# Kernel optimization log

Measured on AMD Instinct MI355X. Metric: run time of the kernel, lower is better.

The kernel has to match this reference:

```python
import jax, jax.numpy as jnp
import numpy as np

EMBED = 1024
HEADS = 16
HEAD_DIM = EMBED // HEADS
N, L = 2, 2048


def setup_inputs() -> dict:
    key = jax.random.key(0)
    ks = jax.random.split(key, 9)
    s = 0.02
    return {
        "values": jax.random.normal(ks[0], (N, L, EMBED), jnp.float32),
        "key": jax.random.normal(ks[1], (N, L, EMBED), jnp.float32),
        "query": jax.random.normal(ks[2], (N, L, EMBED), jnp.float32),
        "mask": jnp.ones((N, 1, 1, L), jnp.int32),
        "Wv": jax.random.normal(ks[3], (HEAD_DIM, HEAD_DIM), jnp.float32) * s,
        "Wk": jax.random.normal(ks[4], (HEAD_DIM, HEAD_DIM), jnp.float32) * s,
        "Wq": jax.random.normal(ks[5], (HEAD_DIM, HEAD_DIM), jnp.float32) * s,
        "bq": jax.random.normal(ks[6], (HEAD_DIM,), jnp.float32) * s,
        "Wo": jax.random.normal(ks[7], (EMBED, EMBED), jnp.float32) * s,
        "bo": jax.random.normal(ks[8], (EMBED,), jnp.float32) * s,
    }


def reference(values, key, query, mask, Wv, Wk, Wq, bq, Wo, bo):
    n, q_len, E = query.shape
    D = Wv.shape[0]
    H = E // D
    # split heads: (N, len, H, D)
    v = values.reshape(n, -1, H, D)
    k = key.reshape(n, -1, H, D)
    q = query.reshape(n, q_len, H, D)
    # per-head linear projections (torch Linear: x @ W.T [+ b])
    v = jnp.einsum("nlhd,ed->nlhe", v, Wv)
    k = jnp.einsum("nlhd,ed->nlhe", k, Wk)
    q = jnp.einsum("nlhd,ed->nlhe", q, Wq) + bq
    # scores: (N, H, q_len, k_len)
    energy = jnp.einsum("nqhd,nkhd->nhqk", q, k)
    energy = jnp.where(mask == 0, jnp.float32(-1e20), energy)
    # NOTE: original scales by sqrt(embed_size), not sqrt(head_dim)
    attn = jax.nn.softmax(energy / jnp.sqrt(jnp.float32(E)), axis=-1)
    out = jnp.einsum("nhqk,nkhd->nqhd", attn, v).reshape(n, q_len, E)
    return out @ Wo.T + bo
```

## Files before the change

### kernel.cpp

```cpp
#include <hip/hip_runtime.h>
#include <hip/hip_bf16.h>
#include <string.h>

#define NB   2
#define SEQ  2048
#define EMB  1024
#define NH   16
#define HD   64
#define QSCALE 0.045084219f

typedef __attribute__((ext_vector_type(8))) short short8;
typedef __attribute__((ext_vector_type(4))) float f32x4;

#define MFMA(a, b, c) __builtin_amdgcn_mfma_f32_16x16x32_bf16(a, b, c, 0, 0, 0)
#define EXP2(x) __builtin_amdgcn_exp2f(x)

__device__ __forceinline__ unsigned short f2bf(float x) {
    union { float f; unsigned u; } v; v.f = x;
    unsigned r = v.u + 0x7fffu + ((v.u >> 16) & 1u);
    return (unsigned short)(r >> 16);
}
__device__ __forceinline__ unsigned packbf2(float a, float b) {
    __hip_bfloat162 h = __float22bfloat162_rn(make_float2(a, b));
    unsigned u; memcpy(&u, &h, 4);
    return u;
}
__device__ __forceinline__ void gload16(const void* g, void* l) {
    __builtin_amdgcn_global_load_lds(
        (const __attribute__((address_space(1))) void*)g,
        (__attribute__((address_space(3))) void*)l, 16, 0, 0);
}

__global__ __launch_bounds__(256) void cvt_kernel(
    const float* __restrict__ Wo, const float* __restrict__ Wq,
    const float* __restrict__ Wk, const float* __restrict__ Wv,
    const int* __restrict__ mask,
    unsigned short* __restrict__ Wob, unsigned short* __restrict__ Wqb,
    unsigned short* __restrict__ Wkb, unsigned short* __restrict__ Wvb,
    unsigned short* __restrict__ Mb)
{
    const int b = blockIdx.x, tid = threadIdx.x;
    if (b < 1024) {
        int idx = b * 256 + tid;
        float4 w = ((const float4*)Wo)[idx];
        uint2 p; p.x = packbf2(w.x, w.y); p.y = packbf2(w.z, w.w);
        ((uint2*)Wob)[idx] = p;
    } else if (b < 1027) {
        const float* W = (b == 1024) ? Wq : (b == 1025) ? Wk : Wv;
        unsigned short* Wb = (b == 1024) ? Wqb : (b == 1025) ? Wkb : Wvb;
        #pragma unroll
        for (int i = 0; i < 4; ++i) {
            int idx = tid + i * 256;
            float4 w = ((const float4*)W)[idx];
            uint2 p; p.x = packbf2(w.x, w.y); p.y = packbf2(w.z, w.w);
            ((uint2*)Wb)[idx] = p;
        }
    } else {
        #pragma unroll
        for (int i = 0; i < 16; ++i) {
            int idx = tid + i * 256;
            Mb[idx] = mask[idx] ? (unsigned short)0x3F80 : (unsigned short)0;
        }
    }
}

__global__ __launch_bounds__(256) void qkv_kernel(
    const float* __restrict__ Qin, const float* __restrict__ Kin,
    const float* __restrict__ Vin,
    const unsigned short* __restrict__ Wqb, const unsigned short* __restrict__ Wkb,
    const unsigned short* __restrict__ Wvb, const float* __restrict__ bq,
    const int* __restrict__ mask,
    unsigned short* __restrict__ Qp, unsigned short* __restrict__ Kp,
    unsigned short* __restrict__ Vtp)
{
    const int lt = blockIdx.x;
    const int h  = blockIdx.y;
    const int tz = blockIdx.z;
    const int t  = tz >> 1, n = tz & 1;

    const float* X; const unsigned short* Wb;
    if (t == 0)      { X = Qin; Wb = Wqb; }
    else if (t == 1) { X = Kin; Wb = Wkb; }
    else             { X = Vin; Wb = Wvb; }

    __shared__ __align__(16) unsigned short sX[128][70];
    __shared__ __align__(16) unsigned short sT[64][136];

    const int tid = threadIdx.x, wave = tid >> 6, lane = tid & 63;
    const int ln = lane & 15, quad = lane >> 4;

    #pragma unroll
    for (int i = 0; i < 8; ++i) {
        int flat = tid + i * 256;
        int r = flat >> 4, c4 = flat & 15;
        float4 xv = *(const float4*)(X + ((size_t)(n * SEQ + lt * 128 + r)) * EMB + h * HD + c4 * 4);
        uint2 xp; xp.x = packbf2(xv.x, xv.y); xp.y = packbf2(xv.z, xv.w);
        *(uint2*)&sX[r][c4 * 4] = xp;
    }
    short8 wf0[4], wf1[4];
    #pragma unroll
    for (int nt = 0; nt < 4; ++nt) {
        wf0[nt] = *(const short8*)(Wb + (nt * 16 + ln) * HD + quad * 8);
        wf1[nt] = *(const short8*)(Wb + (nt * 16 + ln) * HD + 32 + quad * 8);
    }
    __syncthreads();

    f32x4 acc[2][4];
    #pragma unroll
    for (int set = 0; set < 2; ++set) {
        short8 af0 = *(const short8*)&sX[wave * 32 + set * 16 + ln][quad * 8];
        short8 af1 = *(const short8*)&sX[wave * 32 + set * 16 + ln][32 + quad * 8];
        #pragma unroll
        for (int nt = 0; nt < 4; ++nt) {
            f32x4 a = {0.f, 0.f, 0.f, 0.f};
            a = MFMA(af0, wf0[nt], a);
            a = MFMA(af1, wf1[nt], a);
            acc[set][nt] = a;
        }
    }

    if (t == 0) {
        #pragma unroll
        for (int nt = 0; nt < 4; ++nt) {
            float bb = bq[nt * 16 + ln];
            #pragma unroll
            for (int set = 0; set < 2; ++set)
                #pragma unroll
                for (int a = 0; a < 4; ++a)
                    acc[set][nt][a] = (acc[set][nt][a] + bb) * QSCALE;
        }
    }

    if (t < 2) {
        unsigned short* Out = (t == 0) ? Qp : Kp;
        #pragma unroll
        for (int set = 0; set < 2; ++set)
            #pragma unroll
            for (int a = 0; a < 4; ++a) {
                size_t row = (size_t)((n * NH + h) * SEQ + lt * 128 + wave * 32 + set * 16 + quad * 4 + a);
                #pragma unroll
                for (int nt = 0; nt < 4; ++nt)
                    Out[row * HD + nt * 16 + ln] = f2bf(acc[set][nt][a]);
            }
    } else {
        #pragma unroll
        for (int set = 0; set < 2; ++set)
            #pragma unroll
            for (int a = 0; a < 4; ++a) {
                int l = lt * 128 + wave * 32 + set * 16 + quad * 4 + a;
                if (mask[n * SEQ + l] == 0) {
                    #pragma unroll
                    for (int nt = 0; nt < 4; ++nt) acc[set][nt][a] = 0.f;
                }
            }
        #pragma unroll
        for (int set = 0; set < 2; ++set)
            #pragma unroll
            for (int nt = 0; nt < 4; ++nt)
                #pragma unroll
                for (int a = 0; a < 4; ++a)
                    sT[nt * 16 + ln][wave * 32 + set * 16 + quad * 4 + a] = f2bf(acc[set][nt][a]);
        __syncthreads();
        #pragma unroll
        for (int i = 0; i < 4; ++i) {
            int flat = tid + i * 256;
            int r = flat >> 4, c8 = flat & 15;
            *(float4*)(Vtp + ((size_t)((n * NH + h) * HD + r)) * SEQ + lt * 128 + c8 * 8) =
                *(const float4*)&sT[r][c8 * 8];
        }
    }
}

__global__ __launch_bounds__(256, 2) void flash_kernel(
    const unsigned short* __restrict__ Qp, const unsigned short* __restrict__ Kp,
    const unsigned short* __restrict__ Vtp, const unsigned short* __restrict__ Mb,
    unsigned short* __restrict__ A )
{
    const int nh = blockIdx.x;
    const int qt = blockIdx.y;
    const int n  = nh >> 4, h = nh & 15;

    const int tid  = threadIdx.x;
    const int wave = tid >> 6, lane = tid & 63;
    const int ln   = lane & 15, quad = lane >> 4;
    const int ln7  = lane & 7;

    __shared__ __align__(16) unsigned short Kb[2][64 * 64];
    __shared__ __align__(16) unsigned short Vb[2][64 * 64];
    __shared__ __align__(16) unsigned short sP[4][32 * 64];
    unsigned short* sPw = sP[wave];

    const unsigned short* Qb = Qp + ((size_t)nh * SEQ + qt * 128 + wave * 32) * HD;
    short8 qf[2][2];
    #pragma unroll
    for (int set = 0; set < 2; ++set) {
        qf[set][0] = *(const short8*)(Qb + (set * 16 + ln) * HD + quad * 8);
        qf[set][1] = *(const short8*)(Qb + (set * 16 + ln) * HD + 32 + quad * 8);
    }

    const unsigned short* Kg = Kp  + (size_t)nh * SEQ * HD;
    const unsigned short* Vg = Vtp + (size_t)nh * HD * SEQ;
    const unsigned short* mk = Mb + n * SEQ;

    const int kx0 = ((quad)     ^ ln7) << 3;
    const int kx1 = ((quad + 4) ^ ln7) << 3;
    const int pw0 = ((quad >> 1) ^ ln7) << 3;
    const int pwb = (quad & 1) * 4;

    const int r8  = lane >> 3;
    const int swz = ((lane & 7) ^ r8) << 3;

    f32x4 o[2][4];
    #pragma unroll
    for (int s2 = 0; s2 < 2; ++s2)
        #pragma unroll
        for (int dt = 0; dt < 4; ++dt) o[s2][dt] = (f32x4){0.f, 0.f, 0.f, 0.f};
    f32x4 ol[2] = {(f32x4){0.f, 0.f, 0.f, 0.f}, (f32x4){0.f, 0.f, 0.f, 0.f}};

    #define STAGE(buf, kt_) do {                                                  \
        const unsigned short* kg_ = Kg + ((size_t)((kt_) * 64 + wave * 16 + r8)) * HD + swz; \
        const unsigned short* vg_ = Vg + ((size_t)(wave * 16 + r8)) * SEQ + (kt_) * 64 + swz; \
        unsigned short* kl_ = &Kb[buf][wave * 16 * 64];                           \
        unsigned short* vl_ = &Vb[buf][wave * 16 * 64];                           \
        gload16(kg_,            kl_);                                             \
        gload16(kg_ + 8 * HD,   kl_ + 8 * 64);                                    \
        gload16(vg_,            vl_);                                             \
        gload16(vg_ + 8 * SEQ,  vl_ + 8 * 64);                                    \
    } while (0)

    #define COMPUTE(BUF, KT) do {                                                 \
        short8 mf0 = *(const short8*)(mk + (KT) * 64 + quad * 8);                 \
        short8 mf1 = *(const short8*)(mk + (KT) * 64 + 32 + quad * 8);            \
        _Pragma("unroll")                                                         \
        for (int nt = 0; nt < 4; ++nt) {                                          \
            short8 kf0 = *(const short8*)&Kb[BUF][(nt * 16 + ln) * 64 + kx0];     \
            short8 kf1 = *(const short8*)&Kb[BUF][(nt * 16 + ln) * 64 + kx1];     \
            _Pragma("unroll")                                                     \
            for (int set = 0; set < 2; ++set) {                                   \
                f32x4 z = {0.f, 0.f, 0.f, 0.f};                                   \
                z = MFMA(kf0, qf[set][0], z);                                     \
                z = MFMA(kf1, qf[set][1], z);                                     \
                float p0 = EXP2(z[0]);                                            \
                float p1 = EXP2(z[1]);                                            \
                float p2 = EXP2(z[2]);                                            \
                float p3 = EXP2(z[3]);                                            \
                uint2 w; w.x = packbf2(p0, p1); w.y = packbf2(p2, p3);            \
                *(uint2*)&sPw[(set * 16 + ln) * 64 + (pw0 ^ (nt * 2 << 3)) + pwb] = w; \
            }                                                                     \
        }                                                                         \
        asm volatile("s_waitcnt lgkmcnt(0)" ::: "memory");                        \
        short8 pf[2][2];                                                          \
        _Pragma("unroll")                                                         \
        for (int set = 0; set < 2; ++set) {                                       \
            pf[set][0] = *(const short8*)&sPw[(set * 16 + ln) * 64 + kx0];        \
            pf[set][1] = *(const short8*)&sPw[(set * 16 + ln) * 64 + kx1];        \
        }                                                                         \
        _Pragma("unroll")                                                         \
        for (int set = 0; set < 2; ++set) {                                       \
            ol[set] = MFMA(pf[set][0], mf0, ol[set]);                             \
            ol[set] = MFMA(pf[set][1], mf1, ol[set]);                             \
        }                                                                         \
        _Pragma("unroll")                                                         \
        for (int dt = 0; dt < 4; ++dt) {                                          \
            short8 vf0 = *(const short8*)&Vb[BUF][(dt * 16 + ln) * 64 + kx0];     \
            short8 vf1 = *(const short8*)&Vb[BUF][(dt * 16 + ln) * 64 + kx1];     \
            _Pragma("unroll")                                                     \
            for (int set = 0; set < 2; ++set) {                                   \
                o[set][dt] = MFMA(pf[set][0], vf0, o[set][dt]);                   \
                o[set][dt] = MFMA(pf[set][1], vf1, o[set][dt]);                   \
            }                                                                     \
        }                                                                         \
    } while (0)

    STAGE(0, 0);
    __syncthreads();

    #pragma unroll 1
    for (int kt = 0; kt < SEQ / 64; kt += 2) {
        STAGE(1, kt + 1);
        COMPUTE(0, kt);
        __syncthreads();
        if (kt + 2 < SEQ / 64) STAGE(0, kt + 2);
        COMPUTE(1, kt + 1);
        __syncthreads();
    }
    #undef STAGE
    #undef COMPUTE

    #pragma unroll
    for (int set = 0; set < 2; ++set)
        #pragma unroll
        for (int a = 0; a < 4; ++a) {
            float inv = 1.0f / ol[set][a];
            size_t row = (size_t)(n * SEQ + qt * 128 + wave * 32 + set * 16 + quad * 4 + a);
            #pragma unroll
            for (int dt = 0; dt < 4; ++dt)
                A[row * EMB + h * HD + dt * 16 + ln] = f2bf(o[set][dt][a] * inv);
        }
}

__global__ __launch_bounds__(256) void outproj_kernel(
    const unsigned short* __restrict__ A, const unsigned short* __restrict__ Wob,
    const float* __restrict__ bo, float* __restrict__ Out)
{
    const int ct = blockIdx.x;
    const int rt = blockIdx.y;

    const int tid  = threadIdx.x;
    const int wave = tid >> 6, lane = tid & 63;
    const int ln   = lane & 15, quad = lane >> 4;
    const int ln7  = lane & 7;
    const int wm   = wave >> 1, wn = wave & 1;

    __shared__ __align__(16) unsigned short sA[2][128 * 64];
    __shared__ __align__(16) unsigned short sB[2][128 * 64];

    const int r8  = lane >> 3;
    const int swz = ((lane & 7) ^ r8) << 3;

    f32x4 acc[4][4];
    #pragma unroll
    for (int i = 0; i < 4; ++i)
        #pragma unroll
        for (int j = 0; j < 4; ++j) acc[i][j] = (f32x4){0.f, 0.f, 0.f, 0.f};

    #define STAGE(buf, kc_) do {                                                  \
        _Pragma("unroll")                                                         \
        for (int sub = 0; sub < 4; ++sub) {                                       \
            int rloc = wave * 32 + sub * 8;                                       \
            gload16(A   + (size_t)(rt * 128 + rloc + r8) * EMB + (kc_) * 64 + swz,\
                    &sA[buf][rloc * 64]);                                         \
            gload16(Wob + (size_t)(ct * 128 + rloc + r8) * EMB + (kc_) * 64 + swz,\
                    &sB[buf][rloc * 64]);                                         \
        }                                                                         \
    } while (0)

    #define COMPUTE(BUF) do {                                                     \
        _Pragma("unroll")                                                         \
        for (int ks = 0; ks < 2; ++ks) {                                          \
            short8 af[4], bf[4];                                                  \
            _Pragma("unroll")                                                     \
            for (int i = 0; i < 4; ++i)                                           \
                af[i] = *(const short8*)&sA[BUF][(wm * 64 + i * 16 + ln) * 64     \
                                                + (((ks * 4 + quad) ^ ln7) << 3)];\
            _Pragma("unroll")                                                     \
            for (int j = 0; j < 4; ++j)                                           \
                bf[j] = *(const short8*)&sB[BUF][(wn * 64 + j * 16 + ln) * 64     \
                                                + (((ks * 4 + quad) ^ ln7) << 3)];\
            _Pragma("unroll")                                                     \
            for (int i = 0; i < 4; ++i)                                           \
                _Pragma("unroll")                                                 \
                for (int j = 0; j < 4; ++j)                                       \
                    acc[i][j] = MFMA(af[i], bf[j], acc[i][j]);                    \
        }                                                                         \
    } while (0)

    STAGE(0, 0);
    __syncthreads();

    #pragma unroll 1
    for (int kc = 0; kc < EMB / 64; kc += 2) {
        STAGE(1, kc + 1);
        COMPUTE(0);
        __syncthreads();
        if (kc + 2 < EMB / 64) STAGE(0, kc + 2);
        COMPUTE(1);
        __syncthreads();
    }
    #undef STAGE
    #undef COMPUTE

    #pragma unroll
    for (int j = 0; j < 4; ++j) {
        int col = ct * 128 + wn * 64 + j * 16 + ln;
        float bb = bo[col];
        #pragma unroll
        for (int i = 0; i < 4; ++i)
            #pragma unroll
            for (int a = 0; a < 4; ++a) {
                size_t row = (size_t)(rt * 128 + wm * 64 + i * 16 + quad * 4 + a);
                Out[row * EMB + col] = acc[i][j][a] + bb;
            }
    }
}

extern "C" void kernel_launch(void* const* d_in, const int* in_sizes, int n_in,
                              void* d_out, int out_size, void* d_ws, size_t ws_size,
                              hipStream_t stream) {
    const float* values = (const float*)d_in[0];
    const float* key_   = (const float*)d_in[1];
    const float* query  = (const float*)d_in[2];
    const int*   mask   = (const int*)d_in[3];
    const float* Wv     = (const float*)d_in[4];
    const float* Wk     = (const float*)d_in[5];
    const float* Wq     = (const float*)d_in[6];
    const float* bq     = (const float*)d_in[7];
    const float* Wo     = (const float*)d_in[8];
    const float* bo     = (const float*)d_in[9];
    float* out = (float*)d_out;

    const size_t NHLD = (size_t)NB * NH * SEQ * HD;

    unsigned short* ws = (unsigned short*)d_ws;
    unsigned short* Qp    = ws;
    unsigned short* Kp    = ws + NHLD;
    unsigned short* Vtp   = ws + 2 * NHLD;
    unsigned short* Aattn = ws + 3 * NHLD;
    unsigned short* Wob   = ws + 4 * NHLD;
    unsigned short* Wqb   = Wob + (size_t)EMB * EMB;
    unsigned short* Wkb   = Wqb + HD * HD;
    unsigned short* Wvb   = Wkb + HD * HD;
    unsigned short* Mb    = Wvb + HD * HD;

    cvt_kernel<<<dim3(1028), 256, 0, stream>>>(
        Wo, Wq, Wk, Wv, mask, Wob, Wqb, Wkb, Wvb, Mb);
    qkv_kernel<<<dim3(SEQ / 128, NH, 3 * NB), 256, 0, stream>>>(
        query, key_, values, Wqb, Wkb, Wvb, bq, mask, Qp, Kp, Vtp);
    flash_kernel<<<dim3(NB * NH, SEQ / 128), 256, 0, stream>>>(
        Qp, Kp, Vtp, Mb, Aattn);
    outproj_kernel<<<dim3(EMB / 128, NB * SEQ / 128), 256, 0, stream>>>(
        Aattn, Wob, bo, out);
}
```

Baseline: 185.4 us.

## Fuse weight/mask conversion into QKV kernel, stage Q/K stores, raise MFMA priority

Removes the separate cvt_kernel launch. Its Wo and mask conversion moves into the first blocks of qkv_kernel, and the small per-head weights are now converted from fp32 directly inside each QKV block. The Q/K outputs are first staged through shared memory so they can be written as coalesced 16-byte stores, replacing scattered 2-byte stores. The flash kernel raises wave priority around its PV MFMA section. The aim is to save a launch and improve store efficiency, at the cost of extra per-block weight conversion work and more shared memory.

```diff
diff --git a/kernel.cpp b/kernel.cpp
--- a/kernel.cpp
+++ b/kernel.cpp
@@ -25,51 +25,25 @@
     unsigned u; memcpy(&u, &h, 4);
     return u;
 }
+__device__ __forceinline__ short8 pack8(float4 a, float4 b) {
+    unsigned u[4];
+    u[0] = packbf2(a.x, a.y); u[1] = packbf2(a.z, a.w);
+    u[2] = packbf2(b.x, b.y); u[3] = packbf2(b.z, b.w);
+    short8 r; memcpy(&r, u, 16); return r;
+}
 __device__ __forceinline__ void gload16(const void* g, void* l) {
     __builtin_amdgcn_global_load_lds(
         (const __attribute__((address_space(1))) void*)g,
         (__attribute__((address_space(3))) void*)l, 16, 0, 0);
 }
 
-__global__ __launch_bounds__(256) void cvt_kernel(
-    const float* __restrict__ Wo, const float* __restrict__ Wq,
-    const float* __restrict__ Wk, const float* __restrict__ Wv,
-    const int* __restrict__ mask,
-    unsigned short* __restrict__ Wob, unsigned short* __restrict__ Wqb,
-    unsigned short* __restrict__ Wkb, unsigned short* __restrict__ Wvb,
-    unsigned short* __restrict__ Mb)
-{
-    const int b = blockIdx.x, tid = threadIdx.x;
-    if (b < 1024) {
-        int idx = b * 256 + tid;
-        float4 w = ((const float4*)Wo)[idx];
-        uint2 p; p.x = packbf2(w.x, w.y); p.y = packbf2(w.z, w.w);
-        ((uint2*)Wob)[idx] = p;
-    } else if (b < 1027) {
-        const float* W = (b == 1024) ? Wq : (b == 1025) ? Wk : Wv;
-        unsigned short* Wb = (b == 1024) ? Wqb : (b == 1025) ? Wkb : Wvb;
-        #pragma unroll
-        for (int i = 0; i < 4; ++i) {
-            int idx = tid + i * 256;
-            float4 w = ((const float4*)W)[idx];
-            uint2 p; p.x = packbf2(w.x, w.y); p.y = packbf2(w.z, w.w);
-            ((uint2*)Wb)[idx] = p;
-        }
-    } else {
-        #pragma unroll
-        for (int i = 0; i < 16; ++i) {
-            int idx = tid + i * 256;
-            Mb[idx] = mask[idx] ? (unsigned short)0x3F80 : (unsigned short)0;
-        }
-    }
-}
-
 __global__ __launch_bounds__(256) void qkv_kernel(
     const float* __restrict__ Qin, const float* __restrict__ Kin,
     const float* __restrict__ Vin,
-    const unsigned short* __restrict__ Wqb, const unsigned short* __restrict__ Wkb,
-    const unsigned short* __restrict__ Wvb, const float* __restrict__ bq,
-    const int* __restrict__ mask,
+    const float* __restrict__ Wqf, const float* __restrict__ Wkf,
+    const float* __restrict__ Wvf, const float* __restrict__ bq,
+    const int* __restrict__ mask, const float* __restrict__ Wo,
+    unsigned short* __restrict__ Wob, unsigned short* __restrict__ Mb,
     unsigned short* __restrict__ Qp, unsigned short* __restrict__ Kp,
     unsigned short* __restrict__ Vtp)
 {
@@ -77,17 +51,30 @@
     const int h  = blockIdx.y;
     const int tz = blockIdx.z;
     const int t  = tz >> 1, n = tz & 1;
-
-    const float* X; const unsigned short* Wb;
-    if (t == 0)      { X = Qin; Wb = Wqb; }
-    else if (t == 1) { X = Kin; Wb = Wkb; }
-    else             { X = Vin; Wb = Wvb; }
-
-    __shared__ __align__(16) unsigned short sX[128][70];
-    __shared__ __align__(16) unsigned short sT[64][136];
+    const int bid = blockIdx.x + 16 * blockIdx.y + 256 * blockIdx.z;
 
     const int tid = threadIdx.x, wave = tid >> 6, lane = tid & 63;
     const int ln = lane & 15, quad = lane >> 4;
+
+    if (bid < 1024) {
+        int idx = bid * 256 + tid;
+        float4 w = ((const float4*)Wo)[idx];
+        uint2 p; p.x = packbf2(w.x, w.y); p.y = packbf2(w.z, w.w);
+        ((uint2*)Wob)[idx] = p;
+    } else if (bid < 1040) {
+        int idx = (bid - 1024) * 256 + tid;
+        Mb[idx] = mask[idx] ? (unsigned short)0x3F80 : (unsigned short)0;
+    }
+
+    const float* X; const float* Wf;
+    if (t == 0)      { X = Qin; Wf = Wqf; }
+    else if (t == 1) { X = Kin; Wf = Wkf; }
+    else             { X = Vin; Wf = Wvf; }
+
+    __shared__ __align__(16) unsigned short sX[128][70];
+    __shared__ __align__(16) unsigned short sPool[128 * 72];
+    unsigned short (*sT)[136] = (unsigned short(*)[136])sPool;
+    unsigned short (*sM)[72]  = (unsigned short(*)[72])sPool;
 
     #pragma unroll
     for (int i = 0; i < 8; ++i) {
@@ -100,8 +87,11 @@
     short8 wf0[4], wf1[4];
     #pragma unroll
     for (int nt = 0; nt < 4; ++nt) {
-        wf0[nt] = *(const short8*)(Wb + (nt * 16 + ln) * HD + quad * 8);
-        wf1[nt] = *(const short8*)(Wb + (nt * 16 + ln) * HD + 32 + quad * 8);
+        const float* wr = Wf + (nt * 16 + ln) * HD;
+        wf0[nt] = pack8(*(const float4*)(wr + quad * 8),
+                        *(const float4*)(wr + quad * 8 + 4));
+        wf1[nt] = pack8(*(const float4*)(wr + 32 + quad * 8),
+                        *(const float4*)(wr + 32 + quad * 8 + 4));
     }
     __syncthreads();
 
@@ -132,16 +122,24 @@
     }
 
     if (t < 2) {
+        #pragma unroll
+        for (int set = 0; set < 2; ++set)
+            #pragma unroll
+            for (int nt = 0; nt < 4; ++nt)
+                #pragma unroll
+                for (int a = 0; a < 4; ++a)
+                    sM[wave * 32 + set * 16 + quad * 4 + a][nt * 16 + ln] =
+                        f2bf(acc[set][nt][a]);
+        __syncthreads();
         unsigned short* Out = (t == 0) ? Qp : Kp;
-        #pragma unroll
-        for (int set = 0; set < 2; ++set)
-            #pragma unroll
-            for (int a = 0; a < 4; ++a) {
-                size_t row = (size_t)((n * NH + h) * SEQ + lt * 128 + wave * 32 + set * 16 + quad * 4 + a);
-                #pragma unroll
-                for (int nt = 0; nt < 4; ++nt)
-                    Out[row * HD + nt * 16 + ln] = f2bf(acc[set][nt][a]);
-            }
+        size_t base = ((size_t)((n * NH + h) * SEQ + lt * 128)) * HD;
+        #pragma unroll
+        for (int i = 0; i < 4; ++i) {
+            int idx = tid + i * 256;
+            int r = idx >> 3, c8 = idx & 7;
+            *(float4*)(Out + base + (size_t)r * HD + c8 * 8) =
+                *(const float4*)&sM[r][c8 * 8];
+        }
     } else {
         #pragma unroll
         for (int set = 0; set < 2; ++set)
@@ -249,6 +247,7 @@
             }                                                                     \
         }                                                                         \
         asm volatile("s_waitcnt lgkmcnt(0)" ::: "memory");                        \
+        __builtin_amdgcn_s_setprio(1);                                            \
         short8 pf[2][2];                                                          \
         _Pragma("unroll")                                                         \
         for (int set = 0; set < 2; ++set) {                                       \
@@ -270,6 +269,7 @@
                 o[set][dt] = MFMA(pf[set][1], vf1, o[set][dt]);                   \
             }                                                                     \
         }                                                                         \
+        __builtin_amdgcn_s_setprio(0);                                            \
     } while (0)
 
     STAGE(0, 0);
@@ -407,15 +407,10 @@
     unsigned short* Vtp   = ws + 2 * NHLD;
     unsigned short* Aattn = ws + 3 * NHLD;
     unsigned short* Wob   = ws + 4 * NHLD;
-    unsigned short* Wqb   = Wob + (size_t)EMB * EMB;
-    unsigned short* Wkb   = Wqb + HD * HD;
-    unsigned short* Wvb   = Wkb + HD * HD;
-    unsigned short* Mb    = Wvb + HD * HD;
-
-    cvt_kernel<<<dim3(1028), 256, 0, stream>>>(
-        Wo, Wq, Wk, Wv, mask, Wob, Wqb, Wkb, Wvb, Mb);
+    unsigned short* Mb    = Wob + (size_t)EMB * EMB;
+
     qkv_kernel<<<dim3(SEQ / 128, NH, 3 * NB), 256, 0, stream>>>(
-        query, key_, values, Wqb, Wkb, Wvb, bq, mask, Qp, Kp, Vtp);
+        query, key_, values, Wq, Wk, Wv, bq, mask, Wo, Wob, Mb, Qp, Kp, Vtp);
     flash_kernel<<<dim3(NB * NH, SEQ / 128), 256, 0, stream>>>(
         Qp, Kp, Vtp, Mb, Aattn);
     outproj_kernel<<<dim3(EMB / 128, NB * SEQ / 128), 256, 0, stream>>>(
```

Result: no change. 188.3 us (+1.5%).

## Software-pipeline flash loop: overlap P·V of previous tile with QK of next

Applied to the files above, without the earlier changes.

The attention inner loop is split into QK (scores, exp, write P to LDS), VFLOAD (V fragments into registers) and PV (mask-sum and P·V MFMAs) stages. It is restructured so each iteration runs PV for the previous key tile while computing QK for the next, with double-buffered P scratch in LDS and two register sets of V fragments. This removes the explicit LDS wait between writing P and reading it back, and exposes independent MFMA and exp work to hide latency. The cost is higher register use (two sets of V fragments) and double the LDS for P, which could reduce occupancy or cause spills.

```diff
diff --git a/kernel.cpp b/kernel.cpp
--- a/kernel.cpp
+++ b/kernel.cpp
@@ -187,8 +187,9 @@
 
     __shared__ __align__(16) unsigned short Kb[2][64 * 64];
     __shared__ __align__(16) unsigned short Vb[2][64 * 64];
-    __shared__ __align__(16) unsigned short sP[4][32 * 64];
-    unsigned short* sPw = sP[wave];
+    __shared__ __align__(16) unsigned short sP[2][4][32 * 64];
+    unsigned short* const sPw0 = &sP[0][wave][0];
+    unsigned short* const sPw1 = &sP[1][wave][0];
 
     const unsigned short* Qb = Qp + ((size_t)nh * SEQ + qt * 128 + wave * 32) * HD;
     short8 qf[2][2];
@@ -216,6 +217,8 @@
         #pragma unroll
         for (int dt = 0; dt < 4; ++dt) o[s2][dt] = (f32x4){0.f, 0.f, 0.f, 0.f};
     f32x4 ol[2] = {(f32x4){0.f, 0.f, 0.f, 0.f}, (f32x4){0.f, 0.f, 0.f, 0.f}};
+
+    short8 vfA[4][2], vfB[4][2];
 
     #define STAGE(buf, kt_) do {                                                  \
         const unsigned short* kg_ = Kg + ((size_t)((kt_) * 64 + wave * 16 + r8)) * HD + swz; \
@@ -228,13 +231,11 @@
         gload16(vg_ + 8 * SEQ,  vl_ + 8 * 64);                                    \
     } while (0)
 
-    #define COMPUTE(BUF, KT) do {                                                 \
-        short8 mf0 = *(const short8*)(mk + (KT) * 64 + quad * 8);                 \
-        short8 mf1 = *(const short8*)(mk + (KT) * 64 + 32 + quad * 8);            \
+    #define QK(SPW, KBUF, KT) do {                                               \
         _Pragma("unroll")                                                         \
         for (int nt = 0; nt < 4; ++nt) {                                          \
-            short8 kf0 = *(const short8*)&Kb[BUF][(nt * 16 + ln) * 64 + kx0];     \
-            short8 kf1 = *(const short8*)&Kb[BUF][(nt * 16 + ln) * 64 + kx1];     \
+            short8 kf0 = *(const short8*)&Kb[KBUF][(nt * 16 + ln) * 64 + kx0];    \
+            short8 kf1 = *(const short8*)&Kb[KBUF][(nt * 16 + ln) * 64 + kx1];    \
             _Pragma("unroll")                                                     \
             for (int set = 0; set < 2; ++set) {                                   \
                 f32x4 z = {0.f, 0.f, 0.f, 0.f};                                   \
@@ -245,15 +246,27 @@
                 float p2 = EXP2(z[2]);                                            \
                 float p3 = EXP2(z[3]);                                            \
                 uint2 w; w.x = packbf2(p0, p1); w.y = packbf2(p2, p3);            \
-                *(uint2*)&sPw[(set * 16 + ln) * 64 + (pw0 ^ (nt * 2 << 3)) + pwb] = w; \
+                *(uint2*)&(SPW)[(set * 16 + ln) * 64 + (pw0 ^ (nt * 2 << 3)) + pwb] = w; \
             }                                                                     \
         }                                                                         \
-        asm volatile("s_waitcnt lgkmcnt(0)" ::: "memory");                        \
+    } while (0)
+
+    #define VFLOAD(VF, VBUF) do {                                                 \
+        _Pragma("unroll")                                                         \
+        for (int dt = 0; dt < 4; ++dt) {                                          \
+            (VF)[dt][0] = *(const short8*)&Vb[VBUF][(dt * 16 + ln) * 64 + kx0];   \
+            (VF)[dt][1] = *(const short8*)&Vb[VBUF][(dt * 16 + ln) * 64 + kx1];   \
+        }                                                                         \
+    } while (0)
+
+    #define PV(SPW, VF, KT) do {                                                  \
+        short8 mf0 = *(const short8*)(mk + (KT) * 64 + quad * 8);                 \
+        short8 mf1 = *(const short8*)(mk + (KT) * 64 + 32 + quad * 8);            \
         short8 pf[2][2];                                                          \
         _Pragma("unroll")                                                         \
         for (int set = 0; set < 2; ++set) {                                       \
-            pf[set][0] = *(const short8*)&sPw[(set * 16 + ln) * 64 + kx0];        \
-            pf[set][1] = *(const short8*)&sPw[(set * 16 + ln) * 64 + kx1];        \
+            pf[set][0] = *(const short8*)&(SPW)[(set * 16 + ln) * 64 + kx0];      \
+            pf[set][1] = *(const short8*)&(SPW)[(set * 16 + ln) * 64 + kx1];      \
         }                                                                         \
         _Pragma("unroll")                                                         \
         for (int set = 0; set < 2; ++set) {                                       \
@@ -262,30 +275,45 @@
         }                                                                         \
         _Pragma("unroll")                                                         \
         for (int dt = 0; dt < 4; ++dt) {                                          \
-            short8 vf0 = *(const short8*)&Vb[BUF][(dt * 16 + ln) * 64 + kx0];     \
-            short8 vf1 = *(const short8*)&Vb[BUF][(dt * 16 + ln) * 64 + kx1];     \
             _Pragma("unroll")                                                     \
             for (int set = 0; set < 2; ++set) {                                   \
-                o[set][dt] = MFMA(pf[set][0], vf0, o[set][dt]);                   \
-                o[set][dt] = MFMA(pf[set][1], vf1, o[set][dt]);                   \
+                o[set][dt] = MFMA(pf[set][0], (VF)[dt][0], o[set][dt]);           \
+                o[set][dt] = MFMA(pf[set][1], (VF)[dt][1], o[set][dt]);           \
             }                                                                     \
         }                                                                         \
     } while (0)
 
     STAGE(0, 0);
     __syncthreads();
+    STAGE(1, 1);
+    QK(sPw0, 0, 0);
+    VFLOAD(vfA, 0);
+    __syncthreads();
 
     #pragma unroll 1
-    for (int kt = 0; kt < SEQ / 64; kt += 2) {
-        STAGE(1, kt + 1);
-        COMPUTE(0, kt);
+    for (int m = 0; m < 15; ++m) {
+        const int i1 = 2 * m + 1;
+        STAGE(0, i1 + 1);
+        PV(sPw0, vfA, i1 - 1);
+        QK(sPw1, 1, i1);
+        VFLOAD(vfB, 1);
         __syncthreads();
-        if (kt + 2 < SEQ / 64) STAGE(0, kt + 2);
-        COMPUTE(1, kt + 1);
+        STAGE(1, i1 + 2);
+        PV(sPw1, vfB, i1);
+        QK(sPw0, 0, i1 + 1);
+        VFLOAD(vfA, 0);
         __syncthreads();
     }
+    PV(sPw0, vfA, 30);
+    QK(sPw1, 1, 31);
+    VFLOAD(vfB, 1);
+    __syncthreads();
+    PV(sPw1, vfB, 31);
+
     #undef STAGE
-    #undef COMPUTE
+    #undef QK
+    #undef VFLOAD
+    #undef PV
 
     #pragma unroll
     for (int set = 0; set < 2; ++set)
```

Measured after the change: 189.4 us. 2.1% more time.
